# Kernel optimization log

Hardware: AMD Instinct MI355X
Metric: run time of the kernel (lower is better)

## Reference

```python
import jax, jax.numpy as jnp
import numpy as np

EMB_DIM = 256
HEAD_DIM = 32


def setup_inputs() -> dict:
    key = jax.random.key(0)
    kx, kq, kk, kv = jax.random.split(key, 4)
    B, S = 4, 4096
    x = jax.random.normal(kx, (B, S, EMB_DIM), dtype=jnp.float32)
    # Linear(emb_dim, head_dim, bias=False): store as [emb_dim, head_dim]
    sc = 1.0 / np.sqrt(EMB_DIM)
    Wq = jax.random.normal(kq, (EMB_DIM, HEAD_DIM), dtype=jnp.float32) * sc
    Wk = jax.random.normal(kk, (EMB_DIM, HEAD_DIM), dtype=jnp.float32) * sc
    Wv = jax.random.normal(kv, (EMB_DIM, HEAD_DIM), dtype=jnp.float32) * sc
    return {"x": x, "Wq": Wq, "Wk": Wk, "Wv": Wv}


def reference(x, Wq, Wk, Wv):
    # single-head attention with POST-softmax scaling (as in source).
    # Dropout treated as identity (eval mode) for determinism.
    scaling = HEAD_DIM ** (-0.5)
    q = jnp.einsum('bse,ed->bsd', x, Wq)
    k = jnp.einsum('bse,ed->bsd', x, Wk)
    v = jnp.einsum('bse,ed->bsd', x, Wv)
    energy = jnp.einsum('bqd,bkd->bqk', q, k)  # [B,S,S]
    att = jax.nn.softmax(energy, axis=-1) * scaling
    out = jnp.einsum('bqk,bkd->bqd', att, v)
    return out
```

## Files before the change

kernel.cpp:

```cpp
#include <hip/hip_runtime.h>

#define EMB 256
#define HD 32
#define SEQ 4096
#define NSPLIT 8
#define KRANGE 512
#define NQROW 16384

typedef _Float16 half8 __attribute__((ext_vector_type(8)));
typedef _Float16 half4v __attribute__((ext_vector_type(4)));
typedef float floatx4 __attribute__((ext_vector_type(4)));

#define L2E 1.44269504088896340736f
#define SCALING 0.17677669529663687f

__device__ __forceinline__ void xpose2(unsigned x, unsigned y, unsigned& o0, unsigned& o1) {
  int lane = threadIdx.x & 63;
  int n = lane & 15, quad = lane >> 4;
  int a0 = (n + 32 * (quad & 1)) << 2;
  int a1 = (n + 16 + 32 * (quad & 1)) << 2;
  unsigned t0 = (unsigned)__builtin_amdgcn_ds_bpermute(a0, (int)x);
  unsigned t1 = (unsigned)__builtin_amdgcn_ds_bpermute(a0, (int)y);
  o0 = (quad < 2) ? t0 : t1;
  unsigned t2 = (unsigned)__builtin_amdgcn_ds_bpermute(a1, (int)x);
  unsigned t3 = (unsigned)__builtin_amdgcn_ds_bpermute(a1, (int)y);
  o1 = (quad < 2) ? t2 : t3;
}

__device__ __forceinline__ float crossmax(float x) {
  x = fmaxf(x, __shfl_xor(x, 16));
  return fmaxf(x, __shfl_xor(x, 32));
}

__device__ __forceinline__ half8 mk8(unsigned a, unsigned b, unsigned c, unsigned d) {
  union { unsigned u[4]; half8 h; } z;
  z.u[0] = a; z.u[1] = b; z.u[2] = c; z.u[3] = d;
  return z.h;
}

__global__ __launch_bounds__(256) void prep_kernel(const float* __restrict__ Wq,
                                                   const float* __restrict__ Wk,
                                                   const float* __restrict__ Wv,
                                                   _Float16* __restrict__ wsw) {
  int gid = blockIdx.x * 256 + threadIdx.x;
  int j    = gid & 7;
  int lane = (gid >> 3) & 63;
  int kc   = (gid >> 9) & 7;
  int half = (gid >> 12) & 1;
  int mat  = gid >> 13;
  const float* W = (mat == 0) ? Wq : ((mat == 1) ? Wk : Wv);
  int n = lane & 15, quad = lane >> 4;
  int e = kc * 32 + quad * 8 + j;
  int d = n + half * 16;
  float v = W[e * HD + d];
  if (mat == 0) v *= L2E;
  wsw[gid] = (_Float16)v;
}

__global__ __launch_bounds__(256) void qkv_kernel(const float* __restrict__ x,
                                                  const _Float16* __restrict__ wsw,
                                                  _Float16* __restrict__ qw,
                                                  _Float16* __restrict__ kw,
                                                  _Float16* __restrict__ vt) {
  int lane = threadIdx.x & 63, wave = threadIdx.x >> 6;
  int n = lane & 15, quad = lane >> 4;
  int mat = blockIdx.y;
  int rowbase = blockIdx.x * 64 + wave * 16;

  floatx4 c0 = {0,0,0,0}, c1 = {0,0,0,0};

#pragma unroll
  for (int kc = 0; kc < 8; ++kc) {
    const float* xp = x + (rowbase + n) * EMB + kc * 32 + quad * 8;
    float4 xa = *(const float4*)(xp);
    float4 xb = *(const float4*)(xp + 4);
    half8 a;
    a[0] = (_Float16)xa.x; a[1] = (_Float16)xa.y; a[2] = (_Float16)xa.z; a[3] = (_Float16)xa.w;
    a[4] = (_Float16)xb.x; a[5] = (_Float16)xb.y; a[6] = (_Float16)xb.z; a[7] = (_Float16)xb.w;
    half8 b0 = *(const half8*)(wsw + (((mat * 2 + 0) * 8 + kc) << 9) + (lane << 3));
    half8 b1 = *(const half8*)(wsw + (((mat * 2 + 1) * 8 + kc) << 9) + (lane << 3));
    c0 = __builtin_amdgcn_mfma_f32_16x16x32_f16(a, b0, c0, 0, 0, 0);
    c1 = __builtin_amdgcn_mfma_f32_16x16x32_f16(a, b1, c1, 0, 0, 0);
  }

  if (mat == 2) {
    int b = rowbase >> 12;
    int s0 = rowbase & (SEQ - 1);
    _Float16* vb = vt + b * HD * SEQ;
#pragma unroll
    for (int r = 0; r < 4; ++r) {
      int s = s0 + quad * 4 + r;
      vb[n * SEQ + s]        = (_Float16)c0[r];
      vb[(n + 16) * SEQ + s] = (_Float16)c1[r];
    }
  } else {
    _Float16* dst = (mat == 0) ? qw : kw;
#pragma unroll
    for (int r = 0; r < 4; ++r) {
      int row = rowbase + quad * 4 + r;
      dst[row * HD + n]      = (_Float16)c0[r];
      dst[row * HD + n + 16] = (_Float16)c1[r];
    }
  }
}

__global__ __launch_bounds__(256, 4) void attn_kernel(const _Float16* __restrict__ q,
                                                      const _Float16* __restrict__ k,
                                                      const _Float16* __restrict__ vt,
                                                      _Float16* __restrict__ Op,
                                                      float* __restrict__ Mp,
                                                      float* __restrict__ Lp) {
  const int t = threadIdx.x;
  const int w = t >> 6, lane = t & 63;
  const int n = lane & 15, quad = lane >> 4;
  const int qb = blockIdx.x & 127;
  const int sp = blockIdx.x >> 7;
  const int b = qb >> 5;
  const int qrow0 = qb * 128 + w * 32;
  const int key0 = sp * KRANGE;

  const _Float16* kb = k  + (size_t)(b * SEQ + key0) * HD;
  const _Float16* vb = vt + (size_t)b * HD * SEQ + key0;

  half8 qf0 = *(const half8*)(q + (qrow0 + n) * HD + quad * 8);
  half8 qf1 = *(const half8*)(q + (qrow0 + 16 + n) * HD + quad * 8);

  half8 aone = {0,0,0,0,0,0,0,0};
  if (n == 0) { aone[0]=1; aone[1]=1; aone[2]=1; aone[3]=1; aone[4]=1; aone[5]=1; aone[6]=1; aone[7]=1; }

  floatx4 o00 = {0,0,0,0}, o01 = {0,0,0,0};
  floatx4 o10 = {0,0,0,0}, o11 = {0,0,0,0};
  floatx4 l0 = {0,0,0,0}, l1 = {0,0,0,0};
  float m0 = -__builtin_huge_valf(), m1 = -__builtin_huge_valf();
  const floatx4 zero = {0,0,0,0};

#pragma unroll
  for (int kt = 0; kt < KRANGE / 64; ++kt) {
    const _Float16* kt0 = kb + kt * 64 * HD;
    const _Float16* vt0 = vb + kt * 64;
    half8 ka0 = *(const half8*)(kt0 + (n)      * HD + quad * 8);
    half8 ka1 = *(const half8*)(kt0 + (16 + n) * HD + quad * 8);
    half8 ka2 = *(const half8*)(kt0 + (32 + n) * HD + quad * 8);
    half8 ka3 = *(const half8*)(kt0 + (48 + n) * HD + quad * 8);
    half8 va00 = *(const half8*)(vt0 + (n)      * SEQ + quad * 8);
    half8 va01 = *(const half8*)(vt0 + (16 + n) * SEQ + quad * 8);
    half8 va10 = *(const half8*)(vt0 + (n)      * SEQ + 32 + quad * 8);
    half8 va11 = *(const half8*)(vt0 + (16 + n) * SEQ + 32 + quad * 8);

    floatx4 s0[4], s1[4];
    s0[0] = __builtin_amdgcn_mfma_f32_16x16x32_f16(ka0, qf0, zero, 0, 0, 0);
    s0[1] = __builtin_amdgcn_mfma_f32_16x16x32_f16(ka1, qf0, zero, 0, 0, 0);
    s0[2] = __builtin_amdgcn_mfma_f32_16x16x32_f16(ka2, qf0, zero, 0, 0, 0);
    s0[3] = __builtin_amdgcn_mfma_f32_16x16x32_f16(ka3, qf0, zero, 0, 0, 0);
    s1[0] = __builtin_amdgcn_mfma_f32_16x16x32_f16(ka0, qf1, zero, 0, 0, 0);
    s1[1] = __builtin_amdgcn_mfma_f32_16x16x32_f16(ka1, qf1, zero, 0, 0, 0);
    s1[2] = __builtin_amdgcn_mfma_f32_16x16x32_f16(ka2, qf1, zero, 0, 0, 0);
    s1[3] = __builtin_amdgcn_mfma_f32_16x16x32_f16(ka3, qf1, zero, 0, 0, 0);

    half8 B00, B01, B10, B11;
#pragma unroll
    for (int c = 0; c < 2; ++c) {
      floatx4* sv = c ? s1 : s0;
      float& mr = c ? m1 : m0;
      floatx4 t01 = __builtin_elementwise_max(sv[0], sv[1]);
      floatx4 t23 = __builtin_elementwise_max(sv[2], sv[3]);
      floatx4 t4  = __builtin_elementwise_max(t01, t23);
      float mm = fmaxf(fmaxf(t4[0], t4[1]), fmaxf(t4[2], t4[3]));
      mm = crossmax(mm);
      float mnew = fmaxf(mr, mm);
      float alpha = __builtin_amdgcn_exp2f(mr - mnew);
      mr = mnew;

      unsigned pk[4][2];
#pragma unroll
      for (int g = 0; g < 4; ++g) {
        float p0 = __builtin_amdgcn_exp2f(sv[g][0] - mnew);
        float p1 = __builtin_amdgcn_exp2f(sv[g][1] - mnew);
        float p2 = __builtin_amdgcn_exp2f(sv[g][2] - mnew);
        float p3 = __builtin_amdgcn_exp2f(sv[g][3] - mnew);
        pk[g][0] = __builtin_bit_cast(unsigned, __builtin_amdgcn_cvt_pkrtz(p0, p1));
        pk[g][1] = __builtin_bit_cast(unsigned, __builtin_amdgcn_cvt_pkrtz(p2, p3));
      }
      unsigned b00, b02, b01, b03, b10, b12, b11, b13;
      xpose2(pk[0][0], pk[1][0], b00, b02);
      xpose2(pk[0][1], pk[1][1], b01, b03);
      xpose2(pk[2][0], pk[3][0], b10, b12);
      xpose2(pk[2][1], pk[3][1], b11, b13);
      if (c == 0) {
        B00 = mk8(b00, b01, b02, b03); B01 = mk8(b10, b11, b12, b13);
        o00 *= alpha; o01 *= alpha; l0[0] *= alpha;
      } else {
        B10 = mk8(b00, b01, b02, b03); B11 = mk8(b10, b11, b12, b13);
        o10 *= alpha; o11 *= alpha; l1[0] *= alpha;
      }
    }

    o00 = __builtin_amdgcn_mfma_f32_16x16x32_f16(va00, B00, o00, 0, 0, 0);
    o00 = __builtin_amdgcn_mfma_f32_16x16x32_f16(va10, B01, o00, 0, 0, 0);
    o01 = __builtin_amdgcn_mfma_f32_16x16x32_f16(va01, B00, o01, 0, 0, 0);
    o01 = __builtin_amdgcn_mfma_f32_16x16x32_f16(va11, B01, o01, 0, 0, 0);
    l0  = __builtin_amdgcn_mfma_f32_16x16x32_f16(aone, B00, l0, 0, 0, 0);
    l0  = __builtin_amdgcn_mfma_f32_16x16x32_f16(aone, B01, l0, 0, 0, 0);

    o10 = __builtin_amdgcn_mfma_f32_16x16x32_f16(va00, B10, o10, 0, 0, 0);
    o10 = __builtin_amdgcn_mfma_f32_16x16x32_f16(va10, B11, o10, 0, 0, 0);
    o11 = __builtin_amdgcn_mfma_f32_16x16x32_f16(va01, B10, o11, 0, 0, 0);
    o11 = __builtin_amdgcn_mfma_f32_16x16x32_f16(va11, B11, o11, 0, 0, 0);
    l1  = __builtin_amdgcn_mfma_f32_16x16x32_f16(aone, B10, l1, 0, 0, 0);
    l1  = __builtin_amdgcn_mfma_f32_16x16x32_f16(aone, B11, l1, 0, 0, 0);
  }

  half4v p00, p01, p10, p11;
#pragma unroll
  for (int r = 0; r < 4; ++r) {
    p00[r] = (_Float16)o00[r]; p01[r] = (_Float16)o01[r];
    p10[r] = (_Float16)o10[r]; p11[r] = (_Float16)o11[r];
  }
  size_t obase = ((size_t)(sp * NQROW + qrow0)) * 32;
  *(half4v*)&Op[obase + (size_t)n * 32 + quad * 4]             = p00;
  *(half4v*)&Op[obase + (size_t)n * 32 + 16 + quad * 4]        = p01;
  *(half4v*)&Op[obase + (size_t)(16 + n) * 32 + quad * 4]      = p10;
  *(half4v*)&Op[obase + (size_t)(16 + n) * 32 + 16 + quad * 4] = p11;
  if (quad == 0) {
    int mi = sp * NQROW + qrow0;
    Mp[mi + n]      = m0;
    Mp[mi + 16 + n] = m1;
    Lp[mi + n]      = l0[0];
    Lp[mi + 16 + n] = l1[0];
  }
}

__global__ __launch_bounds__(256) void combine_kernel(const _Float16* __restrict__ Op,
                                                      const float* __restrict__ Mp,
                                                      const float* __restrict__ Lp,
                                                      float* __restrict__ out) {
  int gid = blockIdx.x * 256 + threadIdx.x;
  int dc = gid & 7, qrow = gid >> 3;
  float mv[NSPLIT];
  float ms = -__builtin_huge_valf();
#pragma unroll
  for (int sp = 0; sp < NSPLIT; ++sp) {
    mv[sp] = Mp[sp * NQROW + qrow];
    ms = fmaxf(ms, mv[sp]);
  }
  float L = 0.f;
  floatx4 O = {0.f, 0.f, 0.f, 0.f};
#pragma unroll
  for (int sp = 0; sp < NSPLIT; ++sp) {
    float ww = __builtin_amdgcn_exp2f(mv[sp] - ms);
    L += ww * Lp[sp * NQROW + qrow];
    half4v ov = *(const half4v*)&Op[((size_t)(sp * NQROW + qrow)) * 32 + dc * 4];
#pragma unroll
    for (int r = 0; r < 4; ++r) O[r] += ww * (float)ov[r];
  }
  float inv = SCALING / L;
  floatx4 res = {O[0] * inv, O[1] * inv, O[2] * inv, O[3] * inv};
  *(floatx4*)&out[qrow * HD + dc * 4] = res;
}

extern "C" void kernel_launch(void* const* d_in, const int* in_sizes, int n_in,
                              void* d_out, int out_size, void* d_ws, size_t ws_size,
                              hipStream_t stream) {
  const float* x  = (const float*)d_in[0];
  const float* Wq = (const float*)d_in[1];
  const float* Wk = (const float*)d_in[2];
  const float* Wv = (const float*)d_in[3];
  float* out = (float*)d_out;

  _Float16* wsw = (_Float16*)d_ws;
  _Float16* qw  = wsw + 24576;
  _Float16* kw  = qw + NQROW * HD;
  _Float16* vt  = kw + NQROW * HD;
  _Float16* Op  = vt + NQROW * HD;
  float* Mp = (float*)(Op + (size_t)NSPLIT * NQROW * 32);
  float* Lp = Mp + NSPLIT * NQROW;

  prep_kernel<<<96, 256, 0, stream>>>(Wq, Wk, Wv, wsw);
  qkv_kernel<<<dim3(256, 3), 256, 0, stream>>>(x, wsw, qw, kw, vt);
  attn_kernel<<<1024, 256, 0, stream>>>(qw, kw, vt, Op, Mp, Lp);
  combine_kernel<<<512, 256, 0, stream>>>(Op, Mp, Lp, out);
}
```

Baseline: 106.0 us.

## Switch attention inner loop to 32x32x16 MFMA with lane-shuffle P transpose

Rewrites the attention kernel's per-wave tile to use 32x32x16 MFMA instructions, so that one wave handles 32 query rows by 32 keys per step instead of several 16x16 tiles. The score layout puts each query row in one lane pair. The row max and row sum then need only a single xor-32 shuffle, which replaces the bpermute transposes and the extra ones-vector MFMA used for the row sum. The aim is fewer MFMA issues and less cross-lane traffic per key tile. In exchange it uses 32-key steps, which doubles the loop iterations and the rescale frequency, and holds 16-wide accumulators that raise register use.

```diff
diff --git a/kernel.cpp b/kernel.cpp
--- a/kernel.cpp
+++ b/kernel.cpp
@@ -10,27 +10,10 @@
 typedef _Float16 half8 __attribute__((ext_vector_type(8)));
 typedef _Float16 half4v __attribute__((ext_vector_type(4)));
 typedef float floatx4 __attribute__((ext_vector_type(4)));
+typedef float floatx16 __attribute__((ext_vector_type(16)));
 
 #define L2E 1.44269504088896340736f
 #define SCALING 0.17677669529663687f
-
-__device__ __forceinline__ void xpose2(unsigned x, unsigned y, unsigned& o0, unsigned& o1) {
-  int lane = threadIdx.x & 63;
-  int n = lane & 15, quad = lane >> 4;
-  int a0 = (n + 32 * (quad & 1)) << 2;
-  int a1 = (n + 16 + 32 * (quad & 1)) << 2;
-  unsigned t0 = (unsigned)__builtin_amdgcn_ds_bpermute(a0, (int)x);
-  unsigned t1 = (unsigned)__builtin_amdgcn_ds_bpermute(a0, (int)y);
-  o0 = (quad < 2) ? t0 : t1;
-  unsigned t2 = (unsigned)__builtin_amdgcn_ds_bpermute(a1, (int)x);
-  unsigned t3 = (unsigned)__builtin_amdgcn_ds_bpermute(a1, (int)y);
-  o1 = (quad < 2) ? t2 : t3;
-}
-
-__device__ __forceinline__ float crossmax(float x) {
-  x = fmaxf(x, __shfl_xor(x, 16));
-  return fmaxf(x, __shfl_xor(x, 32));
-}
 
 __device__ __forceinline__ half8 mk8(unsigned a, unsigned b, unsigned c, unsigned d) {
   union { unsigned u[4]; half8 h; } z;
@@ -112,7 +95,7 @@
                                                       float* __restrict__ Lp) {
   const int t = threadIdx.x;
   const int w = t >> 6, lane = t & 63;
-  const int n = lane & 15, quad = lane >> 4;
+  const int n2 = lane & 31, h = lane >> 5;
   const int qb = blockIdx.x & 127;
   const int sp = blockIdx.x >> 7;
   const int b = qb >> 5;
@@ -122,111 +105,86 @@
   const _Float16* kb = k  + (size_t)(b * SEQ + key0) * HD;
   const _Float16* vb = vt + (size_t)b * HD * SEQ + key0;
 
-  half8 qf0 = *(const half8*)(q + (qrow0 + n) * HD + quad * 8);
-  half8 qf1 = *(const half8*)(q + (qrow0 + 16 + n) * HD + quad * 8);
-
-  half8 aone = {0,0,0,0,0,0,0,0};
-  if (n == 0) { aone[0]=1; aone[1]=1; aone[2]=1; aone[3]=1; aone[4]=1; aone[5]=1; aone[6]=1; aone[7]=1; }
-
-  floatx4 o00 = {0,0,0,0}, o01 = {0,0,0,0};
-  floatx4 o10 = {0,0,0,0}, o11 = {0,0,0,0};
-  floatx4 l0 = {0,0,0,0}, l1 = {0,0,0,0};
-  float m0 = -__builtin_huge_valf(), m1 = -__builtin_huge_valf();
-  const floatx4 zero = {0,0,0,0};
-
-#pragma unroll
-  for (int kt = 0; kt < KRANGE / 64; ++kt) {
-    const _Float16* kt0 = kb + kt * 64 * HD;
-    const _Float16* vt0 = vb + kt * 64;
-    half8 ka0 = *(const half8*)(kt0 + (n)      * HD + quad * 8);
-    half8 ka1 = *(const half8*)(kt0 + (16 + n) * HD + quad * 8);
-    half8 ka2 = *(const half8*)(kt0 + (32 + n) * HD + quad * 8);
-    half8 ka3 = *(const half8*)(kt0 + (48 + n) * HD + quad * 8);
-    half8 va00 = *(const half8*)(vt0 + (n)      * SEQ + quad * 8);
-    half8 va01 = *(const half8*)(vt0 + (16 + n) * SEQ + quad * 8);
-    half8 va10 = *(const half8*)(vt0 + (n)      * SEQ + 32 + quad * 8);
-    half8 va11 = *(const half8*)(vt0 + (16 + n) * SEQ + 32 + quad * 8);
-
-    floatx4 s0[4], s1[4];
-    s0[0] = __builtin_amdgcn_mfma_f32_16x16x32_f16(ka0, qf0, zero, 0, 0, 0);
-    s0[1] = __builtin_amdgcn_mfma_f32_16x16x32_f16(ka1, qf0, zero, 0, 0, 0);
-    s0[2] = __builtin_amdgcn_mfma_f32_16x16x32_f16(ka2, qf0, zero, 0, 0, 0);
-    s0[3] = __builtin_amdgcn_mfma_f32_16x16x32_f16(ka3, qf0, zero, 0, 0, 0);
-    s1[0] = __builtin_amdgcn_mfma_f32_16x16x32_f16(ka0, qf1, zero, 0, 0, 0);
-    s1[1] = __builtin_amdgcn_mfma_f32_16x16x32_f16(ka1, qf1, zero, 0, 0, 0);
-    s1[2] = __builtin_amdgcn_mfma_f32_16x16x32_f16(ka2, qf1, zero, 0, 0, 0);
-    s1[3] = __builtin_amdgcn_mfma_f32_16x16x32_f16(ka3, qf1, zero, 0, 0, 0);
-
-    half8 B00, B01, B10, B11;
-#pragma unroll
-    for (int c = 0; c < 2; ++c) {
-      floatx4* sv = c ? s1 : s0;
-      float& mr = c ? m1 : m0;
-      floatx4 t01 = __builtin_elementwise_max(sv[0], sv[1]);
-      floatx4 t23 = __builtin_elementwise_max(sv[2], sv[3]);
-      floatx4 t4  = __builtin_elementwise_max(t01, t23);
-      float mm = fmaxf(fmaxf(t4[0], t4[1]), fmaxf(t4[2], t4[3]));
-      mm = crossmax(mm);
-      float mnew = fmaxf(mr, mm);
-      float alpha = __builtin_amdgcn_exp2f(mr - mnew);
-      mr = mnew;
-
-      unsigned pk[4][2];
-#pragma unroll
-      for (int g = 0; g < 4; ++g) {
-        float p0 = __builtin_amdgcn_exp2f(sv[g][0] - mnew);
-        float p1 = __builtin_amdgcn_exp2f(sv[g][1] - mnew);
-        float p2 = __builtin_amdgcn_exp2f(sv[g][2] - mnew);
-        float p3 = __builtin_amdgcn_exp2f(sv[g][3] - mnew);
-        pk[g][0] = __builtin_bit_cast(unsigned, __builtin_amdgcn_cvt_pkrtz(p0, p1));
-        pk[g][1] = __builtin_bit_cast(unsigned, __builtin_amdgcn_cvt_pkrtz(p2, p3));
-      }
-      unsigned b00, b02, b01, b03, b10, b12, b11, b13;
-      xpose2(pk[0][0], pk[1][0], b00, b02);
-      xpose2(pk[0][1], pk[1][1], b01, b03);
-      xpose2(pk[2][0], pk[3][0], b10, b12);
-      xpose2(pk[2][1], pk[3][1], b11, b13);
-      if (c == 0) {
-        B00 = mk8(b00, b01, b02, b03); B01 = mk8(b10, b11, b12, b13);
-        o00 *= alpha; o01 *= alpha; l0[0] *= alpha;
-      } else {
-        B10 = mk8(b00, b01, b02, b03); B11 = mk8(b10, b11, b12, b13);
-        o10 *= alpha; o11 *= alpha; l1[0] *= alpha;
-      }
-    }
-
-    o00 = __builtin_amdgcn_mfma_f32_16x16x32_f16(va00, B00, o00, 0, 0, 0);
-    o00 = __builtin_amdgcn_mfma_f32_16x16x32_f16(va10, B01, o00, 0, 0, 0);
-    o01 = __builtin_amdgcn_mfma_f32_16x16x32_f16(va01, B00, o01, 0, 0, 0);
-    o01 = __builtin_amdgcn_mfma_f32_16x16x32_f16(va11, B01, o01, 0, 0, 0);
-    l0  = __builtin_amdgcn_mfma_f32_16x16x32_f16(aone, B00, l0, 0, 0, 0);
-    l0  = __builtin_amdgcn_mfma_f32_16x16x32_f16(aone, B01, l0, 0, 0, 0);
-
-    o10 = __builtin_amdgcn_mfma_f32_16x16x32_f16(va00, B10, o10, 0, 0, 0);
-    o10 = __builtin_amdgcn_mfma_f32_16x16x32_f16(va10, B11, o10, 0, 0, 0);
-    o11 = __builtin_amdgcn_mfma_f32_16x16x32_f16(va01, B10, o11, 0, 0, 0);
-    o11 = __builtin_amdgcn_mfma_f32_16x16x32_f16(va11, B11, o11, 0, 0, 0);
-    l1  = __builtin_amdgcn_mfma_f32_16x16x32_f16(aone, B10, l1, 0, 0, 0);
-    l1  = __builtin_amdgcn_mfma_f32_16x16x32_f16(aone, B11, l1, 0, 0, 0);
-  }
-
-  half4v p00, p01, p10, p11;
-#pragma unroll
-  for (int r = 0; r < 4; ++r) {
-    p00[r] = (_Float16)o00[r]; p01[r] = (_Float16)o01[r];
-    p10[r] = (_Float16)o10[r]; p11[r] = (_Float16)o11[r];
-  }
-  size_t obase = ((size_t)(sp * NQROW + qrow0)) * 32;
-  *(half4v*)&Op[obase + (size_t)n * 32 + quad * 4]             = p00;
-  *(half4v*)&Op[obase + (size_t)n * 32 + 16 + quad * 4]        = p01;
-  *(half4v*)&Op[obase + (size_t)(16 + n) * 32 + quad * 4]      = p10;
-  *(half4v*)&Op[obase + (size_t)(16 + n) * 32 + 16 + quad * 4] = p11;
-  if (quad == 0) {
-    int mi = sp * NQROW + qrow0;
-    Mp[mi + n]      = m0;
-    Mp[mi + 16 + n] = m1;
-    Lp[mi + n]      = l0[0];
-    Lp[mi + 16 + n] = l1[0];
+  half8 qb0 = *(const half8*)(q + (qrow0 + n2) * HD + h * 8);
+  half8 qb1 = *(const half8*)(q + (qrow0 + n2) * HD + 16 + h * 8);
+
+  floatx16 o;
+#pragma unroll
+  for (int r = 0; r < 16; ++r) o[r] = 0.f;
+  const floatx16 zero16 = o;
+  float m = -__builtin_huge_valf();
+  float l = 0.f;
+
+#pragma unroll
+  for (int kt = 0; kt < KRANGE / 32; ++kt) {
+    const _Float16* kt0 = kb + (kt * 32 + n2) * HD;
+    const _Float16* vt0 = vb + (size_t)n2 * SEQ + kt * 32;
+    half8 ka0 = *(const half8*)(kt0 + h * 8);
+    half8 ka1 = *(const half8*)(kt0 + 16 + h * 8);
+    half8 va0 = *(const half8*)(vt0 + h * 8);
+    half8 va1 = *(const half8*)(vt0 + 16 + h * 8);
+
+    floatx16 s = __builtin_amdgcn_mfma_f32_32x32x16_f16(ka0, qb0, zero16, 0, 0, 0);
+    s = __builtin_amdgcn_mfma_f32_32x32x16_f16(ka1, qb1, s, 0, 0, 0);
+
+    floatx4 s0 = {s[0], s[1], s[2], s[3]};
+    floatx4 s1 = {s[4], s[5], s[6], s[7]};
+    floatx4 s2 = {s[8], s[9], s[10], s[11]};
+    floatx4 s3 = {s[12], s[13], s[14], s[15]};
+    floatx4 t01 = __builtin_elementwise_max(s0, s1);
+    floatx4 t23 = __builtin_elementwise_max(s2, s3);
+    floatx4 t4  = __builtin_elementwise_max(t01, t23);
+    float mm = fmaxf(fmaxf(t4[0], t4[1]), fmaxf(t4[2], t4[3]));
+    mm = fmaxf(mm, __shfl_xor(mm, 32));
+    float mnew = fmaxf(m, mm);
+    float alpha = __builtin_amdgcn_exp2f(m - mnew);
+    m = mnew;
+
+    float p[16];
+#pragma unroll
+    for (int r = 0; r < 16; ++r) p[r] = __builtin_amdgcn_exp2f(s[r] - mnew);
+    unsigned pk[8];
+#pragma unroll
+    for (int g = 0; g < 8; ++g)
+      pk[g] = __builtin_bit_cast(unsigned, __builtin_amdgcn_cvt_pkrtz(p[2 * g], p[2 * g + 1]));
+
+    float ps = ((p[0] + p[1]) + (p[2] + p[3])) + ((p[4] + p[5]) + (p[6] + p[7]))
+             + ((p[8] + p[9]) + (p[10] + p[11])) + ((p[12] + p[13]) + (p[14] + p[15]));
+    ps += __shfl_xor(ps, 32);
+    l = l * alpha + ps;
+
+#pragma unroll
+    for (int r = 0; r < 16; ++r) o[r] *= alpha;
+
+    unsigned tmp0 = h ? pk[0] : pk[2];
+    unsigned tmp1 = h ? pk[1] : pk[3];
+    unsigned tmp2 = h ? pk[4] : pk[6];
+    unsigned tmp3 = h ? pk[5] : pk[7];
+    unsigned ex0 = (unsigned)__shfl_xor((int)tmp0, 32);
+    unsigned ex1 = (unsigned)__shfl_xor((int)tmp1, 32);
+    unsigned ex2 = (unsigned)__shfl_xor((int)tmp2, 32);
+    unsigned ex3 = (unsigned)__shfl_xor((int)tmp3, 32);
+    half8 B0 = h ? mk8(ex0, ex1, pk[2], pk[3]) : mk8(pk[0], pk[1], ex0, ex1);
+    half8 B1 = h ? mk8(ex2, ex3, pk[6], pk[7]) : mk8(pk[4], pk[5], ex2, ex3);
+
+    o = __builtin_amdgcn_mfma_f32_32x32x16_f16(va0, B0, o, 0, 0, 0);
+    o = __builtin_amdgcn_mfma_f32_32x32x16_f16(va1, B1, o, 0, 0, 0);
+  }
+
+  size_t obase = ((size_t)(sp * NQROW + qrow0) + n2) * 32;
+#pragma unroll
+  for (int bb = 0; bb < 4; ++bb) {
+    half4v pv;
+    pv[0] = (_Float16)o[4 * bb + 0];
+    pv[1] = (_Float16)o[4 * bb + 1];
+    pv[2] = (_Float16)o[4 * bb + 2];
+    pv[3] = (_Float16)o[4 * bb + 3];
+    *(half4v*)&Op[obase + 8 * bb + 4 * h] = pv;
+  }
+  if (h == 0) {
+    int mi = sp * NQROW + qrow0 + n2;
+    Mp[mi] = m;
+    Lp[mi] = l;
   }
 }
 
```

After: 106.9 us. No clear change (+0.8%).
